# Performance work log

Hardware: AMD Instinct MI355X
Metric: run time of the kernel (lower is better)

Reference implementation:

```python
import jax, jax.numpy as jnp
import numpy as np

N = 50000       # nodes
E = 800000      # edges
D_IN, D_H, D_OUT = 64, 64, 32


def _glorot(key, fan_in, fan_out):
    lim = np.sqrt(6.0 / (fan_in + fan_out)).astype(np.float32)
    return jax.random.uniform(key, (fan_in, fan_out), jnp.float32, -lim, lim)


def setup_inputs() -> dict:
    key = jax.random.key(0)
    k = jax.random.split(key, 4)
    x = jax.random.normal(k[0], (N, D_IN), jnp.float32)
    edge_index = jax.random.randint(k[1], (2, E), 0, N, dtype=jnp.int64)
    W1 = _glorot(k[2], D_IN, D_H)
    b1 = jnp.zeros((D_H,), jnp.float32)
    W2 = _glorot(k[3], D_H, D_OUT)
    b2 = jnp.zeros((D_OUT,), jnp.float32)
    return {"x": x, "edge_index": edge_index, "W1": W1, "b1": b1, "W2": W2, "b2": b2}


def gcn_layer(x, W, b, src, dst, n):
    # PyG GCNConv: h = XW; add self-loops (weight 1); symmetric normalization
    # out[j] = sum_{i->j} h[i] / sqrt(deg(i) deg(j)) + h[j]/deg(j) + b
    h = x @ W                                           # [n, d_out]
    deg = jax.ops.segment_sum(jnp.ones((src.shape[0],), h.dtype), dst,
                              num_segments=n) + 1.0     # in-degree + self-loop
    dinv = jax.lax.rsqrt(deg)                           # deg >= 1
    norm = (dinv[src] * dinv[dst])[:, None]             # [E, 1]
    agg = jax.ops.segment_sum(h[src] * norm, dst, num_segments=n)
    # self-loop contribution: dinv[i]*dinv[i]*h[i]
    return agg + h * (dinv * dinv)[:, None] + b


def reference(x, edge_index, W1, b1, W2, b2):
    src, dst = edge_index[0], edge_index[1]
    h = gcn_layer(x, W1, b1, src, dst, N)
    h = jax.nn.relu(h)                                  # dropout is identity in eval mode
    return gcn_layer(h, W2, b2, src, dst, N)
```

## Files before the change

kernel.cpp:

```cpp
#include <hip/hip_runtime.h>
#include <hip/hip_fp16.h>
#include <cstddef>
#include <cstdint>

namespace {

constexpr int N  = 50000;
constexpr int E  = 800000;
constexpr int DH = 64;
constexpr int DO = 32;
constexpr int NB = (N + 255) / 256;
static_assert(N < 65536, "src packed as u16");
static_assert(NB <= 256, "single-tile block scan");

__device__ inline uint16_t f2bf(float f) {
    union { float f; uint32_t u; } c; c.f = f;
    uint32_t r = c.u + 0x7FFFu + ((c.u >> 16) & 1u);
    return (uint16_t)(r >> 16);
}
__device__ inline void bf2x(uint32_t p, float& a, float& b) {
    union { uint32_t u; float f; } c0, c1;
    c0.u = p << 16; c1.u = p & 0xFFFF0000u;
    a = c0.f; b = c1.f;
}

__global__ void k_zero(int* __restrict__ cnt) {
    int i = blockIdx.x * blockDim.x + threadIdx.x;
    if (i < N) cnt[i] = 0;
}

__global__ void k_count(const int* __restrict__ dst, int* __restrict__ cnt,
                        int* __restrict__ rank) {
    int e = blockIdx.x * blockDim.x + threadIdx.x;
    if (e < E) rank[e] = atomicAdd(&cnt[dst[e]], 1);
}

__global__ void k_scanA(const int* __restrict__ cnt, int* __restrict__ incl,
                        int* __restrict__ bsum) {
    __shared__ int ts[256];
    const int t = threadIdx.x;
    const int i = blockIdx.x * 256 + t;
    const int v = (i < N) ? cnt[i] : 0;
    ts[t] = v;
    __syncthreads();
#pragma unroll
    for (int off = 1; off < 256; off <<= 1) {
        const int u = (t >= off) ? ts[t - off] : 0;
        __syncthreads();
        ts[t] += u;
        __syncthreads();
    }
    if (i < N) incl[i] = ts[t];
    if (t == 255) bsum[blockIdx.x] = ts[255];
}

__global__ void k_scanBC(const int* __restrict__ cnt, const int* __restrict__ incl,
                         const int* __restrict__ bsum, int* __restrict__ rowptr,
                         float* __restrict__ dinv) {
    __shared__ int ts[256];
    const int t = threadIdx.x;
    ts[t] = (t < NB) ? bsum[t] : 0;
    __syncthreads();
#pragma unroll
    for (int off = 1; off < 256; off <<= 1) {
        const int u = (t >= off) ? ts[t - off] : 0;
        __syncthreads();
        ts[t] += u;
        __syncthreads();
    }
    const int base = (blockIdx.x == 0) ? 0 : ts[blockIdx.x - 1];
    const int i = blockIdx.x * 256 + t;
    if (i >= N) return;
    const int c    = cnt[i];
    const int excl = base + incl[i] - c;
    rowptr[i] = excl;
    dinv[i]   = rsqrtf((float)(c + 1));
    if (i == N - 1) rowptr[N] = excl + c;
}

__global__ void k_fill(const int* __restrict__ src, const int* __restrict__ dst,
                       const int* __restrict__ rank, const int* __restrict__ rowptr,
                       const float* __restrict__ dinv, uint32_t* __restrict__ epack) {
    int e = blockIdx.x * blockDim.x + threadIdx.x;
    if (e >= E) return;
    const int s = src[e], d = dst[e];
    const int pos = rowptr[d] + rank[e];
    const float wn = dinv[s] * dinv[d];
    const uint16_t hb = __half_as_ushort(__float2half(wn));
    epack[pos] = (uint32_t)s | ((uint32_t)hb << 16);
}

__launch_bounds__(256)
__global__ void k_gemm1(const float* __restrict__ X, const float* __restrict__ W1,
                        uint16_t* __restrict__ h1) {
    __shared__ float Ws[64 * DH];
    __shared__ float Xs[64 * 68];

    const int tid = threadIdx.x;
    const int rowBase = blockIdx.x * 64;

#pragma unroll
    for (int i = 0; i < 4; ++i) {
        const int q = tid + i * 256;
        reinterpret_cast<float4*>(Ws)[q] = reinterpret_cast<const float4*>(W1)[q];
    }
#pragma unroll
    for (int i = 0; i < 4; ++i) {
        const int q   = tid + i * 256;
        const int row = q >> 4;
        const int kq  = q & 15;
        const int gr  = min(rowBase + row, N - 1);
        const float4 v = *reinterpret_cast<const float4*>(X + (size_t)gr * 64 + kq * 4);
        *reinterpret_cast<float4*>(&Xs[row * 68 + kq * 4]) = v;
    }
    __syncthreads();

    const int rg = tid >> 4;
    const int cg = tid & 15;
    float acc[4][4];
#pragma unroll
    for (int r = 0; r < 4; ++r)
#pragma unroll
        for (int c = 0; c < 4; ++c) acc[r][c] = 0.0f;

#pragma unroll
    for (int k4 = 0; k4 < 16; ++k4) {
        const int k = k4 * 4;
        float xr[4][4];
#pragma unroll
        for (int r = 0; r < 4; ++r) {
            const float4 v = *reinterpret_cast<const float4*>(&Xs[(rg * 4 + r) * 68 + k]);
            xr[r][0] = v.x; xr[r][1] = v.y; xr[r][2] = v.z; xr[r][3] = v.w;
        }
#pragma unroll
        for (int i = 0; i < 4; ++i) {
            const float4 v = *reinterpret_cast<const float4*>(&Ws[(k + i) * DH + cg * 4]);
            const float wv[4] = {v.x, v.y, v.z, v.w};
#pragma unroll
            for (int r = 0; r < 4; ++r)
#pragma unroll
                for (int c = 0; c < 4; ++c) acc[r][c] += xr[r][i] * wv[c];
        }
    }

#pragma unroll
    for (int r = 0; r < 4; ++r) {
        const int row = rowBase + rg * 4 + r;
        if (row < N) {
            uint2 o;
            o.x = (uint32_t)f2bf(acc[r][0]) | ((uint32_t)f2bf(acc[r][1]) << 16);
            o.y = (uint32_t)f2bf(acc[r][2]) | ((uint32_t)f2bf(acc[r][3]) << 16);
            *reinterpret_cast<uint2*>(&h1[(size_t)row * DH + cg * 4]) = o;
        }
    }
}

__launch_bounds__(256)
__global__ void k_gemm2(const uint16_t* __restrict__ Y, const float* __restrict__ W2,
                        uint16_t* __restrict__ h2) {
    __shared__ float Ws[64 * DO];
    __shared__ float Xs[64 * 68];

    const int tid = threadIdx.x;
    const int rowBase = blockIdx.x * 64;

#pragma unroll
    for (int i = 0; i < 2; ++i) {
        const int q = tid + i * 256;
        reinterpret_cast<float4*>(Ws)[q] = reinterpret_cast<const float4*>(W2)[q];
    }
#pragma unroll
    for (int i = 0; i < 2; ++i) {
        const int q    = tid + i * 256;
        const int row  = q >> 3;
        const int slot = q & 7;
        const int gr   = min(rowBase + row, N - 1);
        const uint4 v = *reinterpret_cast<const uint4*>(Y + (size_t)gr * DH + slot * 8);
        float f0, f1;
        float4 a, b;
        bf2x(v.x, f0, f1); a.x = f0; a.y = f1;
        bf2x(v.y, f0, f1); a.z = f0; a.w = f1;
        bf2x(v.z, f0, f1); b.x = f0; b.y = f1;
        bf2x(v.w, f0, f1); b.z = f0; b.w = f1;
        *reinterpret_cast<float4*>(&Xs[row * 68 + slot * 8])     = a;
        *reinterpret_cast<float4*>(&Xs[row * 68 + slot * 8 + 4]) = b;
    }
    __syncthreads();

    const int rg = tid >> 4;
    const int cg = tid & 15;
    float acc[4][2];
#pragma unroll
    for (int r = 0; r < 4; ++r) { acc[r][0] = 0.0f; acc[r][1] = 0.0f; }

#pragma unroll
    for (int k4 = 0; k4 < 16; ++k4) {
        const int k = k4 * 4;
        float xr[4][4];
#pragma unroll
        for (int r = 0; r < 4; ++r) {
            const float4 v = *reinterpret_cast<const float4*>(&Xs[(rg * 4 + r) * 68 + k]);
            xr[r][0] = v.x; xr[r][1] = v.y; xr[r][2] = v.z; xr[r][3] = v.w;
        }
#pragma unroll
        for (int i = 0; i < 4; ++i) {
            const float2 v = *reinterpret_cast<const float2*>(&Ws[(k + i) * DO + cg * 2]);
#pragma unroll
            for (int r = 0; r < 4; ++r) {
                acc[r][0] += xr[r][i] * v.x;
                acc[r][1] += xr[r][i] * v.y;
            }
        }
    }

#pragma unroll
    for (int r = 0; r < 4; ++r) {
        const int row = rowBase + rg * 4 + r;
        if (row < N) {
            const uint32_t o = (uint32_t)f2bf(acc[r][0]) | ((uint32_t)f2bf(acc[r][1]) << 16);
            *reinterpret_cast<uint32_t*>(&h2[(size_t)row * DO + cg * 2]) = o;
        }
    }
}

__launch_bounds__(256)
__global__ void k_agg1(const int* __restrict__ rowptr, const uint32_t* __restrict__ epack,
                       const uint16_t* __restrict__ h1, const float* __restrict__ dinv,
                       const float* __restrict__ b1, uint16_t* __restrict__ y1) {
    const int gtid = blockIdx.x * 256 + threadIdx.x;
    const int n    = gtid >> 6;
    const int lane = threadIdx.x & 63;
    if (n >= N) return;
    const int g  = lane >> 3;
    const int sl = lane & 7;
    const int beg = rowptr[n], end = rowptr[n + 1];

    float acc[8] = {0.f, 0.f, 0.f, 0.f, 0.f, 0.f, 0.f, 0.f};
    for (int j = beg; j < end; j += 8) {
        const int jj = j + g;
        int s = 0; float wn = 0.0f;
        if (jj < end) {
            const uint32_t w = epack[jj];
            s  = (int)(w & 0xFFFFu);
            wn = __half2float(__ushort_as_half((uint16_t)(w >> 16)));
        }
        const uint4 v = *reinterpret_cast<const uint4*>(h1 + (size_t)s * DH + sl * 8);
        float f0, f1;
        bf2x(v.x, f0, f1); acc[0] += wn * f0; acc[1] += wn * f1;
        bf2x(v.y, f0, f1); acc[2] += wn * f0; acc[3] += wn * f1;
        bf2x(v.z, f0, f1); acc[4] += wn * f0; acc[5] += wn * f1;
        bf2x(v.w, f0, f1); acc[6] += wn * f0; acc[7] += wn * f1;
    }
#pragma unroll
    for (int m = 8; m < 64; m <<= 1)
#pragma unroll
        for (int k = 0; k < 8; ++k) acc[k] += __shfl_xor(acc[k], m);

    if (g < 2) {
        const float di = dinv[n], d2 = di * di;
        const int fb = sl * 8 + g * 4;
        const uint2 sv = *reinterpret_cast<const uint2*>(h1 + (size_t)n * DH + fb);
        float s0, s1, s2, s3;
        bf2x(sv.x, s0, s1); bf2x(sv.y, s2, s3);
        const float4 bv = *reinterpret_cast<const float4*>(b1 + fb);
        const float o0 = fmaxf(acc[g * 4 + 0] + s0 * d2 + bv.x, 0.f);
        const float o1 = fmaxf(acc[g * 4 + 1] + s1 * d2 + bv.y, 0.f);
        const float o2 = fmaxf(acc[g * 4 + 2] + s2 * d2 + bv.z, 0.f);
        const float o3 = fmaxf(acc[g * 4 + 3] + s3 * d2 + bv.w, 0.f);
        uint2 pk;
        pk.x = (uint32_t)f2bf(o0) | ((uint32_t)f2bf(o1) << 16);
        pk.y = (uint32_t)f2bf(o2) | ((uint32_t)f2bf(o3) << 16);
        *reinterpret_cast<uint2*>(y1 + (size_t)n * DH + fb) = pk;
    }
}

__global__ void k_agg2(const int* __restrict__ rowptr, const uint32_t* __restrict__ epack,
                       const uint16_t* __restrict__ h2, const float* __restrict__ dinv,
                       const float* __restrict__ b2, float* __restrict__ out) {
    const int gtid = blockIdx.x * blockDim.x + threadIdx.x;
    const int n    = gtid >> 6;
    const int lane = gtid & 63;
    if (n >= N) return;
    const int g  = lane >> 2;
    const int sl = lane & 3;
    const int beg = rowptr[n], end = rowptr[n + 1];

    float acc[8] = {0.f, 0.f, 0.f, 0.f, 0.f, 0.f, 0.f, 0.f};
    for (int j = beg; j < end; j += 16) {
        const int jj = j + g;
        int s = 0; float wn = 0.0f;
        if (jj < end) {
            const uint32_t w = epack[jj];
            s  = (int)(w & 0xFFFFu);
            wn = __half2float(__ushort_as_half((uint16_t)(w >> 16)));
        }
        const uint4 v = *reinterpret_cast<const uint4*>(h2 + (size_t)s * DO + sl * 8);
        float f0, f1;
        bf2x(v.x, f0, f1); acc[0] += wn * f0; acc[1] += wn * f1;
        bf2x(v.y, f0, f1); acc[2] += wn * f0; acc[3] += wn * f1;
        bf2x(v.z, f0, f1); acc[4] += wn * f0; acc[5] += wn * f1;
        bf2x(v.w, f0, f1); acc[6] += wn * f0; acc[7] += wn * f1;
    }
#pragma unroll
    for (int m = 4; m < 64; m <<= 1)
#pragma unroll
        for (int k = 0; k < 8; ++k) acc[k] += __shfl_xor(acc[k], m);

    if (g < 2) {
        const float di = dinv[n], d2 = di * di;
        const int fb = sl * 8 + g * 4;
        const uint2 sv = *reinterpret_cast<const uint2*>(h2 + (size_t)n * DO + fb);
        float s0, s1, s2, s3;
        bf2x(sv.x, s0, s1); bf2x(sv.y, s2, s3);
        const float4 bv = *reinterpret_cast<const float4*>(b2 + fb);
        float4 o;
        o.x = acc[g * 4 + 0] + s0 * d2 + bv.x;
        o.y = acc[g * 4 + 1] + s1 * d2 + bv.y;
        o.z = acc[g * 4 + 2] + s2 * d2 + bv.z;
        o.w = acc[g * 4 + 3] + s3 * d2 + bv.w;
        *reinterpret_cast<float4*>(out + (size_t)n * DO + fb) = o;
    }
}

template <typename T>
T* alignp(char*& p, size_t count) {
    uintptr_t u = ((uintptr_t)p + 63) & ~(uintptr_t)63;
    p = (char*)(u + count * sizeof(T));
    return (T*)u;
}

}

extern "C" void kernel_launch(void* const* d_in, const int* in_sizes, int n_in,
                              void* d_out, int out_size, void* d_ws, size_t ws_size,
                              hipStream_t stream) {
    const float* x   = (const float*)d_in[0];
    const int*   ei  = (const int*)d_in[1];
    const float* W1  = (const float*)d_in[2];
    const float* b1  = (const float*)d_in[3];
    const float* W2  = (const float*)d_in[4];
    const float* b2  = (const float*)d_in[5];
    float* out = (float*)d_out;

    const int* src = ei;
    const int* dst = ei + E;

    char* p = (char*)d_ws;
    int*      cnt    = alignp<int>(p, N);
    int*      rowptr = alignp<int>(p, N + 1);
    int*      rank   = alignp<int>(p, E);
    float*    dinv   = alignp<float>(p, N);
    int*      incl   = alignp<int>(p, N);
    int*      bsum   = alignp<int>(p, NB);
    uint32_t* epack  = alignp<uint32_t>(p, E);
    uint16_t* h1     = alignp<uint16_t>(p, (size_t)N * DH);
    uint16_t* y1     = alignp<uint16_t>(p, (size_t)N * DH);
    uint16_t* h2     = alignp<uint16_t>(p, (size_t)N * DO);

    hipLaunchKernelGGL(k_zero, dim3((N + 255) / 256), dim3(256), 0, stream, cnt);
    hipLaunchKernelGGL(k_count, dim3((E + 255) / 256), dim3(256), 0, stream,
                       dst, cnt, rank);
    hipLaunchKernelGGL(k_gemm1, dim3((N + 63) / 64), dim3(256), 0, stream, x, W1, h1);
    hipLaunchKernelGGL(k_scanA, dim3(NB), dim3(256), 0, stream, cnt, incl, bsum);
    hipLaunchKernelGGL(k_scanBC, dim3(NB), dim3(256), 0, stream,
                       cnt, incl, bsum, rowptr, dinv);
    hipLaunchKernelGGL(k_fill, dim3((E + 255) / 256), dim3(256), 0, stream,
                       src, dst, rank, rowptr, dinv, epack);
    hipLaunchKernelGGL(k_agg1, dim3((N * 64 + 255) / 256), dim3(256), 0, stream,
                       rowptr, epack, h1, dinv, b1, y1);
    hipLaunchKernelGGL(k_gemm2, dim3((N + 63) / 64), dim3(256), 0, stream, y1, W2, h2);
    hipLaunchKernelGGL(k_agg2, dim3((N * 64 + 255) / 256), dim3(256), 0, stream,
                       rowptr, epack, h2, dinv, b2, out);
}
```

Measured before the change: 151.1 us.

## Fuse CSR preprocessing kernels into one cooperative kernel with grid syncs

```diff
diff --git a/kernel.cpp b/kernel.cpp
--- a/kernel.cpp
+++ b/kernel.cpp
@@ -1,4 +1,5 @@
 #include <hip/hip_runtime.h>
+#include <hip/hip_cooperative_groups.h>
 #include <hip/hip_fp16.h>
 #include <cstddef>
 #include <cstdint>
@@ -10,8 +11,10 @@
 constexpr int DH = 64;
 constexpr int DO = 32;
 constexpr int NB = (N + 255) / 256;
+constexpr int PREB = 1024;
 static_assert(N < 65536, "src packed as u16");
 static_assert(NB <= 256, "single-tile block scan");
+static_assert(NB <= PREB, "scan tiles fit in coop grid");
 
 __device__ inline uint16_t f2bf(float f) {
     union { float f; uint32_t u; } c; c.f = f;
@@ -24,70 +27,71 @@
     a = c0.f; b = c1.f;
 }
 
-__global__ void k_zero(int* __restrict__ cnt) {
-    int i = blockIdx.x * blockDim.x + threadIdx.x;
-    if (i < N) cnt[i] = 0;
-}
-
-__global__ void k_count(const int* __restrict__ dst, int* __restrict__ cnt,
-                        int* __restrict__ rank) {
-    int e = blockIdx.x * blockDim.x + threadIdx.x;
-    if (e < E) rank[e] = atomicAdd(&cnt[dst[e]], 1);
-}
-
-__global__ void k_scanA(const int* __restrict__ cnt, int* __restrict__ incl,
-                        int* __restrict__ bsum) {
+__launch_bounds__(256)
+__global__ void k_pre(const int* __restrict__ src, const int* __restrict__ dst,
+                      int* __restrict__ cnt, int* __restrict__ rank,
+                      int* __restrict__ incl, int* __restrict__ bsum,
+                      int* __restrict__ rowptr, float* __restrict__ dinv,
+                      uint32_t* __restrict__ epack) {
+    namespace cg = cooperative_groups;
+    cg::grid_group grid = cg::this_grid();
+    const int T   = PREB * 256;
+    const int tid = blockIdx.x * 256 + threadIdx.x;
     __shared__ int ts[256];
-    const int t = threadIdx.x;
-    const int i = blockIdx.x * 256 + t;
-    const int v = (i < N) ? cnt[i] : 0;
-    ts[t] = v;
-    __syncthreads();
-#pragma unroll
-    for (int off = 1; off < 256; off <<= 1) {
-        const int u = (t >= off) ? ts[t - off] : 0;
+
+    for (int i = tid; i < N; i += T) cnt[i] = 0;
+    grid.sync();
+
+    for (int e = tid; e < E; e += T) rank[e] = atomicAdd(&cnt[dst[e]], 1);
+    grid.sync();
+
+    if (blockIdx.x < NB) {
+        const int t = threadIdx.x;
+        const int i = blockIdx.x * 256 + t;
+        ts[t] = (i < N) ? cnt[i] : 0;
         __syncthreads();
-        ts[t] += u;
+#pragma unroll
+        for (int off = 1; off < 256; off <<= 1) {
+            const int u = (t >= off) ? ts[t - off] : 0;
+            __syncthreads();
+            ts[t] += u;
+            __syncthreads();
+        }
+        if (i < N) incl[i] = ts[t];
+        if (t == 255) bsum[blockIdx.x] = ts[255];
+    }
+    grid.sync();
+
+    if (blockIdx.x < NB) {
+        const int t = threadIdx.x;
+        ts[t] = (t < NB) ? bsum[t] : 0;
         __syncthreads();
-    }
-    if (i < N) incl[i] = ts[t];
-    if (t == 255) bsum[blockIdx.x] = ts[255];
-}
-
-__global__ void k_scanBC(const int* __restrict__ cnt, const int* __restrict__ incl,
-                         const int* __restrict__ bsum, int* __restrict__ rowptr,
-                         float* __restrict__ dinv) {
-    __shared__ int ts[256];
-    const int t = threadIdx.x;
-    ts[t] = (t < NB) ? bsum[t] : 0;
-    __syncthreads();
-#pragma unroll
-    for (int off = 1; off < 256; off <<= 1) {
-        const int u = (t >= off) ? ts[t - off] : 0;
-        __syncthreads();
-        ts[t] += u;
-        __syncthreads();
-    }
-    const int base = (blockIdx.x == 0) ? 0 : ts[blockIdx.x - 1];
-    const int i = blockIdx.x * 256 + t;
-    if (i >= N) return;
-    const int c    = cnt[i];
-    const int excl = base + incl[i] - c;
-    rowptr[i] = excl;
-    dinv[i]   = rsqrtf((float)(c + 1));
-    if (i == N - 1) rowptr[N] = excl + c;
-}
-
-__global__ void k_fill(const int* __restrict__ src, const int* __restrict__ dst,
-                       const int* __restrict__ rank, const int* __restrict__ rowptr,
-                       const float* __restrict__ dinv, uint32_t* __restrict__ epack) {
-    int e = blockIdx.x * blockDim.x + threadIdx.x;
-    if (e >= E) return;
-    const int s = src[e], d = dst[e];
-    const int pos = rowptr[d] + rank[e];
-    const float wn = dinv[s] * dinv[d];
-    const uint16_t hb = __half_as_ushort(__float2half(wn));
-    epack[pos] = (uint32_t)s | ((uint32_t)hb << 16);
+#pragma unroll
+        for (int off = 1; off < 256; off <<= 1) {
+            const int u = (t >= off) ? ts[t - off] : 0;
+            __syncthreads();
+            ts[t] += u;
+            __syncthreads();
+        }
+        const int base = (blockIdx.x == 0) ? 0 : ts[blockIdx.x - 1];
+        const int i = blockIdx.x * 256 + t;
+        if (i < N) {
+            const int c    = cnt[i];
+            const int excl = base + incl[i] - c;
+            rowptr[i] = excl;
+            dinv[i]   = rsqrtf((float)(c + 1));
+            if (i == N - 1) rowptr[N] = excl + c;
+        }
+    }
+    grid.sync();
+
+    for (int e = tid; e < E; e += T) {
+        const int s = src[e], d = dst[e];
+        const int pos = rowptr[d] + rank[e];
+        const float wn = dinv[s] * dinv[d];
+        const uint16_t hb = __half_as_ushort(__float2half(wn));
+        epack[pos] = (uint32_t)s | ((uint32_t)hb << 16);
+    }
 }
 
 __launch_bounds__(256)
@@ -357,15 +361,12 @@
     uint16_t* y1     = alignp<uint16_t>(p, (size_t)N * DH);
     uint16_t* h2     = alignp<uint16_t>(p, (size_t)N * DO);
 
-    hipLaunchKernelGGL(k_zero, dim3((N + 255) / 256), dim3(256), 0, stream, cnt);
-    hipLaunchKernelGGL(k_count, dim3((E + 255) / 256), dim3(256), 0, stream,
-                       dst, cnt, rank);
+    void* args[] = {(void*)&src, (void*)&dst, (void*)&cnt, (void*)&rank,
+                    (void*)&incl, (void*)&bsum, (void*)&rowptr, (void*)&dinv,
+                    (void*)&epack};
+    hipLaunchCooperativeKernel((const void*)k_pre, dim3(PREB), dim3(256),
+                               args, 0, stream);
     hipLaunchKernelGGL(k_gemm1, dim3((N + 63) / 64), dim3(256), 0, stream, x, W1, h1);
-    hipLaunchKernelGGL(k_scanA, dim3(NB), dim3(256), 0, stream, cnt, incl, bsum);
-    hipLaunchKernelGGL(k_scanBC, dim3(NB), dim3(256), 0, stream,
-                       cnt, incl, bsum, rowptr, dinv);
-    hipLaunchKernelGGL(k_fill, dim3((E + 255) / 256), dim3(256), 0, stream,
-                       src, dst, rank, rowptr, dinv, epack);
     hipLaunchKernelGGL(k_agg1, dim3((N * 64 + 255) / 256), dim3(256), 0, stream,
                        rowptr, epack, h1, dinv, b1, y1);
     hipLaunchKernelGGL(k_gemm2, dim3((N + 63) / 64), dim3(256), 0, stream, y1, W2, h2);
```

New measurement: 521.5 us. 245% more time.
